# Optimization experiments

Measured on AMD Instinct MI355X. Metric: run time of the kernel, lower is better.

The kernel has to match this reference:

```python
import jax, jax.numpy as jnp
import numpy as np

N = 100000      # nodes
E = 1600000     # edges (avg degree 16)
D_IN, D_H1, D_H2, D_OUT = 512, 256, 256, 64


def setup_inputs() -> dict:
    key = jax.random.key(0)
    ks = jax.random.split(key, 8)
    x = jax.random.normal(ks[0], (N, D_IN), dtype=jnp.float32)
    row = jax.random.randint(ks[1], (E,), 0, N, dtype=jnp.int32)
    col = jax.random.randint(ks[2], (E,), 0, N, dtype=jnp.int32)
    vals = jax.random.uniform(ks[3], (E,), dtype=jnp.float32)
    # xavier-normal-ish scaling for weights
    W1 = jax.random.normal(ks[4], (D_IN, D_H1), dtype=jnp.float32) * np.sqrt(2.0 / (D_IN + D_H1))
    W2 = jax.random.normal(ks[5], (D_H1, D_H2), dtype=jnp.float32) * np.sqrt(2.0 / (D_H1 + D_H2))
    W3 = jax.random.normal(ks[6], (D_H2, D_OUT), dtype=jnp.float32) * np.sqrt(2.0 / (D_H2 + D_OUT))
    b1 = jnp.zeros((D_H1,), dtype=jnp.float32)
    b2 = jnp.zeros((D_H2,), dtype=jnp.float32)
    b3 = jnp.zeros((D_OUT,), dtype=jnp.float32)
    return {"x": x, "row": row, "col": col, "vals": vals,
            "W1": W1, "b1": b1, "W2": W2, "b2": b2, "W3": W3, "b3": b3}


def reference(x, row, col, vals, W1, b1, W2, b2, W3, b3):
    n = x.shape[0]

    def spmm(h):
        # out[i] = sum_{e: row[e]==i} vals[e] * h[col[e]]  (COO spmm)
        return jax.ops.segment_sum(vals[:, None] * h[col], row, num_segments=n)

    # layer 1: linear -> spmm -> relu  (dropout p=0 -> identity)
    h = jax.nn.relu(spmm(x @ W1 + b1))
    # layer 2
    h = jax.nn.relu(spmm(h @ W2 + b2))
    # output layer: no activation, no dropout
    return spmm(h @ W3 + b3)
```

## Files before the change

### kernel.cpp

```cpp
#include <hip/hip_runtime.h>

typedef _Float16 f16;
typedef _Float16 f16x4 __attribute__((ext_vector_type(4)));
typedef _Float16 f16x8 __attribute__((ext_vector_type(8)));
typedef float f32x4 __attribute__((ext_vector_type(4)));

#define DEVI __device__ __forceinline__

static constexpr int CAP = 64;

DEVI f16x8 cvt8(float4 a, float4 b) {
  f16x8 r;
  r[0] = (f16)a.x; r[1] = (f16)a.y; r[2] = (f16)a.z; r[3] = (f16)a.w;
  r[4] = (f16)b.x; r[5] = (f16)b.y; r[6] = (f16)b.z; r[7] = (f16)b.w;
  return r;
}

__global__ __launch_bounds__(256)
void prep_w(const float* __restrict__ W1, const float* __restrict__ W2,
            const float* __restrict__ W3, f16* __restrict__ WT1,
            f16* __restrict__ WT2, f16* __restrict__ WT3) {
  int t = blockIdx.x * 256 + threadIdx.x;
  const float* W; f16* O; int N; int u;
  if (t < 16384) {
    W = W1; O = WT1; N = 256; u = t;
  } else if (t < 16384 + 8192) {
    W = W2; O = WT2; N = 256; u = t - 16384;
  } else if (t < 16384 + 8192 + 2048) {
    W = W3; O = WT3; N = 64;  u = t - 24576;
  } else return;
  const int per = (N >> 4) * 64;
  const int kc = u / per;
  const int rem = u - kc * per;
  const int l = rem & 63;
  const int n = ((rem >> 6) << 4) + (l & 15);
  const int kb = kc * 32 + ((l >> 4) << 3);
  f16x8 o;
#pragma unroll
  for (int j = 0; j < 8; ++j) o[j] = (f16)W[(size_t)(kb + j) * N + n];
  *(f16x8*)(O + (size_t)u * 8) = o;
}

__global__ __launch_bounds__(256)
void build_slots(const int* __restrict__ row, const int* __restrict__ col,
                 const float* __restrict__ vals, int* __restrict__ cnt,
                 int2* __restrict__ slots, int E) {
  int e = blockIdx.x * 256 + threadIdx.x;
  if (e >= E) return;
  int r = row[e];
  int p = atomicAdd(&cnt[r], 1);
  if (p < CAP) slots[(size_t)r * CAP + p] = make_int2(col[e], __float_as_int(vals[e]));
}

__global__ __launch_bounds__(256)
void gemm_l1(const float* __restrict__ A, const f16* __restrict__ WT,
             const float* __restrict__ bias, f16* __restrict__ C, int M) {
  constexpr int K = 512, N = 256, NF16 = N / 16;
  __shared__ f16 As[64 * 256];

  const int tid = threadIdx.x;
  const int wave = tid >> 6, lane = tid & 63;
  const int quad = lane >> 4, l16 = lane & 15;
  const int r0 = blockIdx.x * 64;

  f32x4 acc[4][4];
#pragma unroll
  for (int mt = 0; mt < 4; ++mt)
#pragma unroll
    for (int nt = 0; nt < 4; ++nt) {
      f32x4 z = {0.f, 0.f, 0.f, 0.f};
      acc[mt][nt] = z;
    }

  for (int kc = 0; kc < 2; ++kc) {
    if (kc) __syncthreads();
#pragma unroll
    for (int it = 0; it < 8; ++it) {
      int i = it * 256 + tid;
      int row = i >> 5, ko = i & 31;
      int grow = min(r0 + row, M - 1);
      const float4* gp = (const float4*)(A + (size_t)grow * K + kc * 256 + ko * 8);
      float4 v0 = gp[0], v1 = gp[1];
      int dst = (row * 512 + ko * 16) ^ ((row & 7) << 4);
      *(f16x8*)((char*)As + dst) = cvt8(v0, v1);
    }
    __syncthreads();
#pragma unroll
    for (int kb = 0; kb < 8; ++kb) {
      f16x8 af[4], bf[4];
#pragma unroll
      for (int mt = 0; mt < 4; ++mt) {
        int row = mt * 16 + l16;
        int src = (row * 512 + kb * 64 + quad * 16) ^ ((row & 7) << 4);
        af[mt] = *(const f16x8*)((char*)As + src);
      }
      const int kg = kc * 8 + kb;
#pragma unroll
      for (int nt = 0; nt < 4; ++nt) {
        int n16 = wave * 4 + nt;
        bf[nt] = *(const f16x8*)(WT + ((size_t)(kg * NF16 + n16) * 64 + lane) * 8);
      }
#pragma unroll
      for (int mt = 0; mt < 4; ++mt)
#pragma unroll
        for (int nt = 0; nt < 4; ++nt)
          acc[mt][nt] = __builtin_amdgcn_mfma_f32_16x16x32_f16(af[mt], bf[nt], acc[mt][nt], 0, 0, 0);
    }
  }

  float bv[4];
#pragma unroll
  for (int nt = 0; nt < 4; ++nt) bv[nt] = bias[wave * 64 + nt * 16 + l16];
#pragma unroll
  for (int mt = 0; mt < 4; ++mt) {
#pragma unroll
    for (int nt = 0; nt < 4; ++nt) {
      int colg = wave * 64 + nt * 16 + l16;
#pragma unroll
      for (int r = 0; r < 4; ++r) {
        int grow = r0 + mt * 16 + quad * 4 + r;
        if (grow < M)
          C[(size_t)grow * N + colg] = (f16)(acc[mt][nt][r] + bv[nt]);
      }
    }
  }
}

template <int NTILES>
__global__ __launch_bounds__(256)
void gemm_direct(const f16* __restrict__ A, const f16* __restrict__ WT,
                 const float* __restrict__ bias, f16* __restrict__ C, int M) {
  constexpr int K = 256, N = NTILES * 64, NF16 = N / 16;
  const int tid = threadIdx.x;
  const int wave = tid >> 6, lane = tid & 63;
  const int quad = lane >> 4, l16 = lane & 15;
  const int gw = blockIdx.x * 4 + wave;
  const int mtile = (NTILES == 1) ? gw : (gw / NTILES);
  const int ntile = (NTILES == 1) ? 0 : (gw % NTILES);
  const int r0 = mtile * 64;
  if (r0 >= M) return;

  size_t arow[4];
#pragma unroll
  for (int mt = 0; mt < 4; ++mt)
    arow[mt] = (size_t)min(r0 + mt * 16 + l16, M - 1) * K;

  f32x4 acc[4][4];
#pragma unroll
  for (int mt = 0; mt < 4; ++mt)
#pragma unroll
    for (int nt = 0; nt < 4; ++nt) {
      f32x4 z = {0.f, 0.f, 0.f, 0.f};
      acc[mt][nt] = z;
    }

#pragma unroll
  for (int kb = 0; kb < 8; ++kb) {
    f16x8 af[4], bf[4];
#pragma unroll
    for (int mt = 0; mt < 4; ++mt)
      af[mt] = *(const f16x8*)(A + arow[mt] + kb * 32 + quad * 8);
#pragma unroll
    for (int nt = 0; nt < 4; ++nt) {
      int n16 = ntile * 4 + nt;
      bf[nt] = *(const f16x8*)(WT + ((size_t)(kb * NF16 + n16) * 64 + lane) * 8);
    }
#pragma unroll
    for (int mt = 0; mt < 4; ++mt)
#pragma unroll
      for (int nt = 0; nt < 4; ++nt)
        acc[mt][nt] = __builtin_amdgcn_mfma_f32_16x16x32_f16(af[mt], bf[nt], acc[mt][nt], 0, 0, 0);
  }

  float bv[4];
#pragma unroll
  for (int nt = 0; nt < 4; ++nt) bv[nt] = bias[ntile * 64 + nt * 16 + l16];
#pragma unroll
  for (int mt = 0; mt < 4; ++mt) {
#pragma unroll
    for (int nt = 0; nt < 4; ++nt) {
      int colg = ntile * 64 + nt * 16 + l16;
#pragma unroll
      for (int r = 0; r < 4; ++r) {
        int grow = r0 + mt * 16 + quad * 4 + r;
        if (grow < M)
          C[(size_t)grow * N + colg] = (f16)(acc[mt][nt][r] + bv[nt]);
      }
    }
  }
}

__global__ __launch_bounds__(256)
void spmm_relu256(const f16* __restrict__ T, const int2* __restrict__ slots,
                  const int* __restrict__ cnt, f16* __restrict__ H, int nrows) {
  const int wave = threadIdx.x >> 6, lane = threadIdx.x & 63;
  const int i = blockIdx.x * 4 + wave;
  if (i >= nrows) return;
  const int c = min(cnt[i], CAP);
  const int2* sl = slots + (size_t)i * CAP;
  float a0 = 0.f, a1 = 0.f, a2 = 0.f, a3 = 0.f;
  int j = 0;
  for (; j + 4 <= c; j += 4) {
    int2 e0 = sl[j], e1 = sl[j + 1], e2 = sl[j + 2], e3 = sl[j + 3];
    f16x4 u0 = ((const f16x4*)(T + (size_t)e0.x * 256))[lane];
    f16x4 u1 = ((const f16x4*)(T + (size_t)e1.x * 256))[lane];
    f16x4 u2 = ((const f16x4*)(T + (size_t)e2.x * 256))[lane];
    f16x4 u3 = ((const f16x4*)(T + (size_t)e3.x * 256))[lane];
    float v0 = __int_as_float(e0.y), v1 = __int_as_float(e1.y);
    float v2 = __int_as_float(e2.y), v3 = __int_as_float(e3.y);
    a0 += v0 * (float)u0.x + v1 * (float)u1.x + v2 * (float)u2.x + v3 * (float)u3.x;
    a1 += v0 * (float)u0.y + v1 * (float)u1.y + v2 * (float)u2.y + v3 * (float)u3.y;
    a2 += v0 * (float)u0.z + v1 * (float)u1.z + v2 * (float)u2.z + v3 * (float)u3.z;
    a3 += v0 * (float)u0.w + v1 * (float)u1.w + v2 * (float)u2.w + v3 * (float)u3.w;
  }
  for (; j < c; ++j) {
    int2 e = sl[j];
    f16x4 u = ((const f16x4*)(T + (size_t)e.x * 256))[lane];
    float v = __int_as_float(e.y);
    a0 += v * (float)u.x; a1 += v * (float)u.y;
    a2 += v * (float)u.z; a3 += v * (float)u.w;
  }
  f16x4 o;
  o.x = (f16)fmaxf(a0, 0.f); o.y = (f16)fmaxf(a1, 0.f);
  o.z = (f16)fmaxf(a2, 0.f); o.w = (f16)fmaxf(a3, 0.f);
  ((f16x4*)(H + (size_t)i * 256))[lane] = o;
}

__global__ __launch_bounds__(256)
void spmm_out64(const f16* __restrict__ T, const int2* __restrict__ slots,
                const int* __restrict__ cnt, float* __restrict__ out, int nrows) {
  const int wave = threadIdx.x >> 6, lane = threadIdx.x & 63;
  const int i = blockIdx.x * 4 + wave;
  if (i >= nrows) return;
  const int c = min(cnt[i], CAP);
  const int2* sl = slots + (size_t)i * CAP;
  float a = 0.f;
  int j = 0;
  for (; j + 4 <= c; j += 4) {
    int2 e0 = sl[j], e1 = sl[j + 1], e2 = sl[j + 2], e3 = sl[j + 3];
    float u0 = (float)T[(size_t)e0.x * 64 + lane];
    float u1 = (float)T[(size_t)e1.x * 64 + lane];
    float u2 = (float)T[(size_t)e2.x * 64 + lane];
    float u3 = (float)T[(size_t)e3.x * 64 + lane];
    a += __int_as_float(e0.y) * u0 + __int_as_float(e1.y) * u1
       + __int_as_float(e2.y) * u2 + __int_as_float(e3.y) * u3;
  }
  for (; j < c; ++j) {
    int2 e = sl[j];
    a += __int_as_float(e.y) * (float)T[(size_t)e.x * 64 + lane];
  }
  out[(size_t)i * 64 + lane] = a;
}

extern "C" void kernel_launch(void* const* d_in, const int* in_sizes, int n_in,
                              void* d_out, int out_size, void* d_ws, size_t ws_size,
                              hipStream_t stream) {
  const float* x    = (const float*)d_in[0];
  const int*   row  = (const int*)d_in[1];
  const int*   col  = (const int*)d_in[2];
  const float* vals = (const float*)d_in[3];
  const float* W1   = (const float*)d_in[4];
  const float* b1   = (const float*)d_in[5];
  const float* W2   = (const float*)d_in[6];
  const float* b2   = (const float*)d_in[7];
  const float* W3   = (const float*)d_in[8];
  const float* b3   = (const float*)d_in[9];
  float* out = (float*)d_out;

  const int N = in_sizes[0] / 512;
  const int E = in_sizes[1];

  char* ws = (char*)d_ws;
  const size_t MiB = 1ull << 20;
  int*  cnt   = (int*)ws;
  int2* slots = (int2*)(ws + 1 * MiB);
  f16*  WT1   = (f16*)(ws + 52 * MiB);
  f16*  WT2   = WT1 + 256 * 512;
  f16*  WT3   = WT2 + 256 * 256;
  f16*  T     = (f16*)(ws + 53 * MiB);
  f16*  H     = (f16*)(ws + 104 * MiB);

  hipMemsetAsync(cnt, 0, (size_t)N * sizeof(int), stream);
  prep_w<<<(16384 + 8192 + 2048 + 255) / 256, 256, 0, stream>>>(W1, W2, W3, WT1, WT2, WT3);
  build_slots<<<(E + 255) / 256, 256, 0, stream>>>(row, col, vals, cnt, slots, E);

  const int mt64 = (N + 63) / 64;
  dim3 gs((N + 3) / 4);

  gemm_l1<<<mt64, 256, 0, stream>>>(x, WT1, b1, T, N);
  spmm_relu256<<<gs, 256, 0, stream>>>(T, slots, cnt, H, N);
  gemm_direct<4><<<mt64, 256, 0, stream>>>(H, WT2, b2, T, N);
  spmm_relu256<<<gs, 256, 0, stream>>>(T, slots, cnt, H, N);
  gemm_direct<1><<<(mt64 + 3) / 4, 256, 0, stream>>>(H, WT3, b3, T, N);
  spmm_out64<<<gs, 256, 0, stream>>>(T, slots, cnt, out, N);
}
```

Measured before the change: 810.5 us.

## Stage GEMM A tiles via global_load_lds, batch spmm gathers, fold memset into prep

Replaces the layer-2/3 GEMMs with kernels that stage the A tile into LDS using direct global-to-LDS loads, so the A rows are shared across waves instead of being re-read by each wave. The layer-3 GEMM now uses 128-row tiles. gemm_l1 splits its staging loop so the global loads are issued before the conversions, with a sched_barrier between them. spmm_relu256 processes two rows per wave and issues gathers in batches, and spmm_out64 unrolls by 8, both to raise memory-level parallelism. The count memset is folded into the prep_w launch to drop one API call. Together these add code complexity and raise register and LDS pressure, which may lower occupancy.

```diff
diff --git a/kernel.cpp b/kernel.cpp
--- a/kernel.cpp
+++ b/kernel.cpp
@@ -8,6 +8,12 @@
 #define DEVI __device__ __forceinline__
 
 static constexpr int CAP = 64;
+
+DEVI void g2l16(const void* g, void* l) {
+  __builtin_amdgcn_global_load_lds(
+      (const __attribute__((address_space(1))) void*)g,
+      (__attribute__((address_space(3))) void*)l, 16, 0, 0);
+}
 
 DEVI f16x8 cvt8(float4 a, float4 b) {
   f16x8 r;
@@ -19,8 +25,14 @@
 __global__ __launch_bounds__(256)
 void prep_w(const float* __restrict__ W1, const float* __restrict__ W2,
             const float* __restrict__ W3, f16* __restrict__ WT1,
-            f16* __restrict__ WT2, f16* __restrict__ WT3) {
-  int t = blockIdx.x * 256 + threadIdx.x;
+            f16* __restrict__ WT2, f16* __restrict__ WT3,
+            int* __restrict__ cnt, int Nnodes, int zb) {
+  if ((int)blockIdx.x < zb) {
+    int t = blockIdx.x * 256 + threadIdx.x;
+    if (t < Nnodes) cnt[t] = 0;
+    return;
+  }
+  int t = (blockIdx.x - zb) * 256 + threadIdx.x;
   const float* W; f16* O; int N; int u;
   if (t < 16384) {
     W = W1; O = WT1; N = 256; u = t;
@@ -55,7 +67,7 @@
 __global__ __launch_bounds__(256)
 void gemm_l1(const float* __restrict__ A, const f16* __restrict__ WT,
              const float* __restrict__ bias, f16* __restrict__ C, int M) {
-  constexpr int K = 512, N = 256, NF16 = N / 16;
+  constexpr int K = 512, N = 256;
   __shared__ f16 As[64 * 256];
 
   const int tid = threadIdx.x;
@@ -75,14 +87,24 @@
   for (int kc = 0; kc < 2; ++kc) {
     if (kc) __syncthreads();
 #pragma unroll
-    for (int it = 0; it < 8; ++it) {
-      int i = it * 256 + tid;
-      int row = i >> 5, ko = i & 31;
-      int grow = min(r0 + row, M - 1);
-      const float4* gp = (const float4*)(A + (size_t)grow * K + kc * 256 + ko * 8);
-      float4 v0 = gp[0], v1 = gp[1];
-      int dst = (row * 512 + ko * 16) ^ ((row & 7) << 4);
-      *(f16x8*)((char*)As + dst) = cvt8(v0, v1);
+    for (int half = 0; half < 2; ++half) {
+      float4 v[4][2];
+#pragma unroll
+      for (int it = 0; it < 4; ++it) {
+        int i = (half * 4 + it) * 256 + tid;
+        int row = i >> 5, ko = i & 31;
+        int grow = min(r0 + row, M - 1);
+        const float4* gp = (const float4*)(A + (size_t)grow * K + kc * 256 + ko * 8);
+        v[it][0] = gp[0]; v[it][1] = gp[1];
+      }
+      __builtin_amdgcn_sched_barrier(0);
+#pragma unroll
+      for (int it = 0; it < 4; ++it) {
+        int i = (half * 4 + it) * 256 + tid;
+        int row = i >> 5, ko = i & 31;
+        int dst = (row * 512 + ko * 16) ^ ((row & 7) << 4);
+        *(f16x8*)((char*)As + dst) = cvt8(v[it][0], v[it][1]);
+      }
     }
     __syncthreads();
 #pragma unroll
@@ -96,10 +118,8 @@
       }
       const int kg = kc * 8 + kb;
 #pragma unroll
-      for (int nt = 0; nt < 4; ++nt) {
-        int n16 = wave * 4 + nt;
-        bf[nt] = *(const f16x8*)(WT + ((size_t)(kg * NF16 + n16) * 64 + lane) * 8);
-      }
+      for (int nt = 0; nt < 4; ++nt)
+        bf[nt] = *(const f16x8*)(WT + (size_t)(kg * 16 + wave * 4 + nt) * 512 + lane * 8);
 #pragma unroll
       for (int mt = 0; mt < 4; ++mt)
 #pragma unroll
@@ -126,24 +146,27 @@
   }
 }
 
-template <int NTILES>
-__global__ __launch_bounds__(256)
-void gemm_direct(const f16* __restrict__ A, const f16* __restrict__ WT,
-                 const float* __restrict__ bias, f16* __restrict__ C, int M) {
-  constexpr int K = 256, N = NTILES * 64, NF16 = N / 16;
+__global__ __launch_bounds__(256)
+void gemm_l2(const f16* __restrict__ A, const f16* __restrict__ WT,
+             const float* __restrict__ bias, f16* __restrict__ C, int M) {
+  constexpr int K = 256, N = 256;
+  __shared__ f16 As[64 * 256];
+
   const int tid = threadIdx.x;
   const int wave = tid >> 6, lane = tid & 63;
   const int quad = lane >> 4, l16 = lane & 15;
-  const int gw = blockIdx.x * 4 + wave;
-  const int mtile = (NTILES == 1) ? gw : (gw / NTILES);
-  const int ntile = (NTILES == 1) ? 0 : (gw % NTILES);
-  const int r0 = mtile * 64;
-  if (r0 >= M) return;
-
-  size_t arow[4];
-#pragma unroll
-  for (int mt = 0; mt < 4; ++mt)
-    arow[mt] = (size_t)min(r0 + mt * 16 + l16, M - 1) * K;
+  const int r0 = blockIdx.x * 64;
+
+#pragma unroll
+  for (int s = 0; s < 8; ++s) {
+    int G = wave * 8 + s;
+    int kb = G >> 2, mt = G & 3;
+    int grow = min(r0 + mt * 16 + (lane & 15), M - 1);
+    const f16* gp = A + (size_t)grow * K + kb * 32 + (lane >> 4) * 8;
+    g2l16(gp, &As[G * 512]);
+  }
+  asm volatile("s_waitcnt vmcnt(0)" ::: "memory");
+  __syncthreads();
 
   f32x4 acc[4][4];
 #pragma unroll
@@ -159,12 +182,10 @@
     f16x8 af[4], bf[4];
 #pragma unroll
     for (int mt = 0; mt < 4; ++mt)
-      af[mt] = *(const f16x8*)(A + arow[mt] + kb * 32 + quad * 8);
-#pragma unroll
-    for (int nt = 0; nt < 4; ++nt) {
-      int n16 = ntile * 4 + nt;
-      bf[nt] = *(const f16x8*)(WT + ((size_t)(kb * NF16 + n16) * 64 + lane) * 8);
-    }
+      af[mt] = *(const f16x8*)&As[(size_t)(kb * 4 + mt) * 512 + lane * 8];
+#pragma unroll
+    for (int nt = 0; nt < 4; ++nt)
+      bf[nt] = *(const f16x8*)(WT + (size_t)(kb * 16 + wave * 4 + nt) * 512 + lane * 8);
 #pragma unroll
     for (int mt = 0; mt < 4; ++mt)
 #pragma unroll
@@ -174,12 +195,12 @@
 
   float bv[4];
 #pragma unroll
-  for (int nt = 0; nt < 4; ++nt) bv[nt] = bias[ntile * 64 + nt * 16 + l16];
+  for (int nt = 0; nt < 4; ++nt) bv[nt] = bias[wave * 64 + nt * 16 + l16];
 #pragma unroll
   for (int mt = 0; mt < 4; ++mt) {
 #pragma unroll
     for (int nt = 0; nt < 4; ++nt) {
-      int colg = ntile * 64 + nt * 16 + l16;
+      int colg = wave * 64 + nt * 16 + l16;
 #pragma unroll
       for (int r = 0; r < 4; ++r) {
         int grow = r0 + mt * 16 + quad * 4 + r;
@@ -191,39 +212,162 @@
 }
 
 __global__ __launch_bounds__(256)
+void gemm_l3(const f16* __restrict__ A, const f16* __restrict__ WT,
+             const float* __restrict__ bias, f16* __restrict__ C, int M) {
+  constexpr int K = 256, N = 64;
+  __shared__ f16 As[128 * 256];
+
+  const int tid = threadIdx.x;
+  const int wave = tid >> 6, lane = tid & 63;
+  const int quad = lane >> 4, l16 = lane & 15;
+  const int r0 = blockIdx.x * 128;
+
+#pragma unroll
+  for (int s = 0; s < 16; ++s) {
+    int G = wave * 16 + s;
+    int kb = G >> 3, mt = G & 7;
+    int grow = min(r0 + mt * 16 + (lane & 15), M - 1);
+    const f16* gp = A + (size_t)grow * K + kb * 32 + (lane >> 4) * 8;
+    g2l16(gp, &As[G * 512]);
+  }
+  asm volatile("s_waitcnt vmcnt(0)" ::: "memory");
+  __syncthreads();
+
+  f32x4 acc[2][4];
+#pragma unroll
+  for (int mt = 0; mt < 2; ++mt)
+#pragma unroll
+    for (int nt = 0; nt < 4; ++nt) {
+      f32x4 z = {0.f, 0.f, 0.f, 0.f};
+      acc[mt][nt] = z;
+    }
+
+#pragma unroll
+  for (int kb = 0; kb < 8; ++kb) {
+    f16x8 af[2], bf[4];
+#pragma unroll
+    for (int mt = 0; mt < 2; ++mt)
+      af[mt] = *(const f16x8*)&As[(size_t)(kb * 8 + wave * 2 + mt) * 512 + lane * 8];
+#pragma unroll
+    for (int nt = 0; nt < 4; ++nt)
+      bf[nt] = *(const f16x8*)(WT + (size_t)(kb * 4 + nt) * 512 + lane * 8);
+#pragma unroll
+    for (int mt = 0; mt < 2; ++mt)
+#pragma unroll
+      for (int nt = 0; nt < 4; ++nt)
+        acc[mt][nt] = __builtin_amdgcn_mfma_f32_16x16x32_f16(af[mt], bf[nt], acc[mt][nt], 0, 0, 0);
+  }
+
+  float bv[4];
+#pragma unroll
+  for (int nt = 0; nt < 4; ++nt) bv[nt] = bias[nt * 16 + l16];
+#pragma unroll
+  for (int mt = 0; mt < 2; ++mt) {
+#pragma unroll
+    for (int nt = 0; nt < 4; ++nt) {
+      int colg = nt * 16 + l16;
+#pragma unroll
+      for (int r = 0; r < 4; ++r) {
+        int grow = r0 + wave * 32 + mt * 16 + quad * 4 + r;
+        if (grow < M)
+          C[(size_t)grow * N + colg] = (f16)(acc[mt][nt][r] + bv[nt]);
+      }
+    }
+  }
+}
+
+__global__ __launch_bounds__(256)
 void spmm_relu256(const f16* __restrict__ T, const int2* __restrict__ slots,
                   const int* __restrict__ cnt, f16* __restrict__ H, int nrows) {
   const int wave = threadIdx.x >> 6, lane = threadIdx.x & 63;
-  const int i = blockIdx.x * 4 + wave;
-  if (i >= nrows) return;
-  const int c = min(cnt[i], CAP);
-  const int2* sl = slots + (size_t)i * CAP;
-  float a0 = 0.f, a1 = 0.f, a2 = 0.f, a3 = 0.f;
+  const int i0 = blockIdx.x * 8 + wave * 2;
+  if (i0 >= nrows) return;
+  const bool two = (i0 + 1) < nrows;
+  const int c0 = min(cnt[i0], CAP);
+  const int c1 = two ? min(cnt[i0 + 1], CAP) : 0;
+  const int2* s0 = slots + (size_t)i0 * CAP;
+  const int2* s1 = slots + (size_t)(i0 + 1) * CAP;
+  float a0[4] = {0.f, 0.f, 0.f, 0.f};
+  float a1[4] = {0.f, 0.f, 0.f, 0.f};
   int j = 0;
-  for (; j + 4 <= c; j += 4) {
-    int2 e0 = sl[j], e1 = sl[j + 1], e2 = sl[j + 2], e3 = sl[j + 3];
-    f16x4 u0 = ((const f16x4*)(T + (size_t)e0.x * 256))[lane];
-    f16x4 u1 = ((const f16x4*)(T + (size_t)e1.x * 256))[lane];
-    f16x4 u2 = ((const f16x4*)(T + (size_t)e2.x * 256))[lane];
-    f16x4 u3 = ((const f16x4*)(T + (size_t)e3.x * 256))[lane];
-    float v0 = __int_as_float(e0.y), v1 = __int_as_float(e1.y);
-    float v2 = __int_as_float(e2.y), v3 = __int_as_float(e3.y);
-    a0 += v0 * (float)u0.x + v1 * (float)u1.x + v2 * (float)u2.x + v3 * (float)u3.x;
-    a1 += v0 * (float)u0.y + v1 * (float)u1.y + v2 * (float)u2.y + v3 * (float)u3.y;
-    a2 += v0 * (float)u0.z + v1 * (float)u1.z + v2 * (float)u2.z + v3 * (float)u3.z;
-    a3 += v0 * (float)u0.w + v1 * (float)u1.w + v2 * (float)u2.w + v3 * (float)u3.w;
-  }
-  for (; j < c; ++j) {
-    int2 e = sl[j];
-    f16x4 u = ((const f16x4*)(T + (size_t)e.x * 256))[lane];
-    float v = __int_as_float(e.y);
-    a0 += v * (float)u.x; a1 += v * (float)u.y;
-    a2 += v * (float)u.z; a3 += v * (float)u.w;
-  }
-  f16x4 o;
-  o.x = (f16)fmaxf(a0, 0.f); o.y = (f16)fmaxf(a1, 0.f);
-  o.z = (f16)fmaxf(a2, 0.f); o.w = (f16)fmaxf(a3, 0.f);
-  ((f16x4*)(H + (size_t)i * 256))[lane] = o;
+  const int cmin = min(c0, c1);
+  for (; j + 4 <= cmin; j += 4) {
+    int2 e0[4], e1[4];
+#pragma unroll
+    for (int q = 0; q < 4; ++q) { e0[q] = s0[j + q]; e1[q] = s1[j + q]; }
+    f16x4 u0[4], u1[4];
+#pragma unroll
+    for (int q = 0; q < 4; ++q) {
+      u0[q] = ((const f16x4*)(T + (size_t)e0[q].x * 256))[lane];
+      u1[q] = ((const f16x4*)(T + (size_t)e1[q].x * 256))[lane];
+    }
+#pragma unroll
+    for (int q = 0; q < 4; ++q) {
+      float v0 = __int_as_float(e0[q].y), v1 = __int_as_float(e1[q].y);
+      a0[0] += v0 * (float)u0[q].x; a0[1] += v0 * (float)u0[q].y;
+      a0[2] += v0 * (float)u0[q].z; a0[3] += v0 * (float)u0[q].w;
+      a1[0] += v1 * (float)u1[q].x; a1[1] += v1 * (float)u1[q].y;
+      a1[2] += v1 * (float)u1[q].z; a1[3] += v1 * (float)u1[q].w;
+    }
+  }
+  {
+    int t = j;
+    for (; t + 4 <= c0; t += 4) {
+      int2 e[4];
+#pragma unroll
+      for (int q = 0; q < 4; ++q) e[q] = s0[t + q];
+      f16x4 u[4];
+#pragma unroll
+      for (int q = 0; q < 4; ++q) u[q] = ((const f16x4*)(T + (size_t)e[q].x * 256))[lane];
+#pragma unroll
+      for (int q = 0; q < 4; ++q) {
+        float v = __int_as_float(e[q].y);
+        a0[0] += v * (float)u[q].x; a0[1] += v * (float)u[q].y;
+        a0[2] += v * (float)u[q].z; a0[3] += v * (float)u[q].w;
+      }
+    }
+    for (; t < c0; ++t) {
+      int2 e = s0[t];
+      f16x4 u = ((const f16x4*)(T + (size_t)e.x * 256))[lane];
+      float v = __int_as_float(e.y);
+      a0[0] += v * (float)u.x; a0[1] += v * (float)u.y;
+      a0[2] += v * (float)u.z; a0[3] += v * (float)u.w;
+    }
+  }
+  if (two) {
+    int t = j;
+    for (; t + 4 <= c1; t += 4) {
+      int2 e[4];
+#pragma unroll
+      for (int q = 0; q < 4; ++q) e[q] = s1[t + q];
+      f16x4 u[4];
+#pragma unroll
+      for (int q = 0; q < 4; ++q) u[q] = ((const f16x4*)(T + (size_t)e[q].x * 256))[lane];
+#pragma unroll
+      for (int q = 0; q < 4; ++q) {
+        float v = __int_as_float(e[q].y);
+        a1[0] += v * (float)u[q].x; a1[1] += v * (float)u[q].y;
+        a1[2] += v * (float)u[q].z; a1[3] += v * (float)u[q].w;
+      }
+    }
+    for (; t < c1; ++t) {
+      int2 e = s1[t];
+      f16x4 u = ((const f16x4*)(T + (size_t)e.x * 256))[lane];
+      float v = __int_as_float(e.y);
+      a1[0] += v * (float)u.x; a1[1] += v * (float)u.y;
+      a1[2] += v * (float)u.z; a1[3] += v * (float)u.w;
+    }
+  }
+  f16x4 o0;
+  o0.x = (f16)fmaxf(a0[0], 0.f); o0.y = (f16)fmaxf(a0[1], 0.f);
+  o0.z = (f16)fmaxf(a0[2], 0.f); o0.w = (f16)fmaxf(a0[3], 0.f);
+  ((f16x4*)(H + (size_t)i0 * 256))[lane] = o0;
+  if (two) {
+    f16x4 o1;
+    o1.x = (f16)fmaxf(a1[0], 0.f); o1.y = (f16)fmaxf(a1[1], 0.f);
+    o1.z = (f16)fmaxf(a1[2], 0.f); o1.w = (f16)fmaxf(a1[3], 0.f);
+    ((f16x4*)(H + (size_t)(i0 + 1) * 256))[lane] = o1;
+  }
 }
 
 __global__ __launch_bounds__(256)
@@ -236,14 +380,15 @@
   const int2* sl = slots + (size_t)i * CAP;
   float a = 0.f;
   int j = 0;
-  for (; j + 4 <= c; j += 4) {
-    int2 e0 = sl[j], e1 = sl[j + 1], e2 = sl[j + 2], e3 = sl[j + 3];
-    float u0 = (float)T[(size_t)e0.x * 64 + lane];
-    float u1 = (float)T[(size_t)e1.x * 64 + lane];
-    float u2 = (float)T[(size_t)e2.x * 64 + lane];
-    float u3 = (float)T[(size_t)e3.x * 64 + lane];
-    a += __int_as_float(e0.y) * u0 + __int_as_float(e1.y) * u1
-       + __int_as_float(e2.y) * u2 + __int_as_float(e3.y) * u3;
+  for (; j + 8 <= c; j += 8) {
+    int2 e[8];
+#pragma unroll
+    for (int q = 0; q < 8; ++q) e[q] = sl[j + q];
+    float u[8];
+#pragma unroll
+    for (int q = 0; q < 8; ++q) u[q] = (float)T[(size_t)e[q].x * 64 + lane];
+#pragma unroll
+    for (int q = 0; q < 8; ++q) a += __int_as_float(e[q].y) * u[q];
   }
   for (; j < c; ++j) {
     int2 e = sl[j];
@@ -280,17 +425,17 @@
   f16*  T     = (f16*)(ws + 53 * MiB);
   f16*  H     = (f16*)(ws + 104 * MiB);
 
-  hipMemsetAsync(cnt, 0, (size_t)N * sizeof(int), stream);
-  prep_w<<<(16384 + 8192 + 2048 + 255) / 256, 256, 0, stream>>>(W1, W2, W3, WT1, WT2, WT3);
+  const int zb = (N + 255) / 256;
+  prep_w<<<zb + 104, 256, 0, stream>>>(W1, W2, W3, WT1, WT2, WT3, cnt, N, zb);
   build_slots<<<(E + 255) / 256, 256, 0, stream>>>(row, col, vals, cnt, slots, E);
 
   const int mt64 = (N + 63) / 64;
-  dim3 gs((N + 3) / 4);
+  const int mt128 = (N + 127) / 128;
 
   gemm_l1<<<mt64, 256, 0, stream>>>(x, WT1, b1, T, N);
-  spmm_relu256<<<gs, 256, 0, stream>>>(T, slots, cnt, H, N);
-  gemm_direct<4><<<mt64, 256, 0, stream>>>(H, WT2, b2, T, N);
-  spmm_relu256<<<gs, 256, 0, stream>>>(T, slots, cnt, H, N);
-  gemm_direct<1><<<(mt64 + 3) / 4, 256, 0, stream>>>(H, WT3, b3, T, N);
-  spmm_out64<<<gs, 256, 0, stream>>>(T, slots, cnt, out, N);
-}
+  spmm_relu256<<<(N + 7) / 8, 256, 0, stream>>>(T, slots, cnt, H, N);
+  gemm_l2<<<mt64, 256, 0, stream>>>(H, WT2, b2, T, N);
+  spmm_relu256<<<(N + 7) / 8, 256, 0, stream>>>(T, slots, cnt, H, N);
+  gemm_l3<<<mt128, 256, 0, stream>>>(H, WT3, b3, T, N);
+  spmm_out64<<<(N + 3) / 4, 256, 0, stream>>>(T, slots, cnt, out, N);
+}
```

New measurement: 803.7 us. No clear change (-0.8%).
